# Kernel tuning notes

Measured on AMD Instinct MI355X. Metric: run time of the kernel, lower is better.

Reference implementation:

```python
import jax, jax.numpy as jnp
import numpy as np

IN_CH = 128
OUT_CH = 256
KSIZE = 3
DOWN = 2
WSCALE_GAIN = 1.0
LR_MUL = 1.0
ACT_GAIN = float(np.sqrt(2.0))  # lrelu def_gain
CONV_CLAMP = 256.0
LRELU_SLOPE = 0.2


def _setup_filter():
    # upfirdn2d.setup_filter([1,3,3,1]): normalize 1D then outer product -> 2D
    f1 = jnp.asarray([1.0, 3.0, 3.0, 1.0], dtype=jnp.float32)
    f1 = f1 / jnp.sum(f1)
    f2 = jnp.outer(f1, f1)  # [4,4]
    return f2


def setup_inputs() -> dict:
    key = jax.random.key(0)
    k1, k2 = jax.random.split(key)
    x = jax.random.normal(k1, (16, IN_CH, 256, 256), dtype=jnp.float32)
    weight = jax.random.normal(k2, (OUT_CH, IN_CH, KSIZE, KSIZE), dtype=jnp.float32)
    bias = jnp.zeros((OUT_CH,), dtype=jnp.float32)
    return {"x": x, "weight": weight, "bias": bias}


def reference(x, weight, bias):
    # runtime_gain = 1.0
    fan_in = KSIZE * KSIZE * IN_CH
    wscale = WSCALE_GAIN / np.sqrt(fan_in) * LR_MUL  # use_wscale=True
    w = weight * jnp.float32(wscale)
    b = bias * jnp.float32(LR_MUL)

    # filter_padding for k=3, fh=fw=4, down=2 -> (2,2,2,2) as (left,right,top,bottom)
    pad = (KSIZE // 2 + (4 - DOWN + 1) // 2, KSIZE // 2 + (4 - DOWN) // 2)
    # upfirdn2d(x, f, down=1, padding): pad then correlate with flipped filter
    f2 = _setup_filter()
    f2 = f2[::-1, ::-1]  # flip (symmetric here, kept for faithfulness)
    C = x.shape[1]
    fk = jnp.broadcast_to(f2[None, None], (C, 1, 4, 4))  # depthwise kernel
    x = lax.pad_fn(x, pad) if False else jnp.pad(x, ((0, 0), (0, 0), (pad[1], pad[0]) if False else (pad[0], pad[1]), (pad[0], pad[1])))
    x = jax.lax.conv_general_dilated(
        x, fk, window_strides=(1, 1), padding='VALID',
        dimension_numbers=('NCHW', 'OIHW', 'NCHW'),
        feature_group_count=C)

    # strided conv2d, padding=0, stride=down
    x = jax.lax.conv_general_dilated(
        x, w, window_strides=(DOWN, DOWN), padding='VALID',
        dimension_numbers=('NCHW', 'OIHW', 'NCHW'))

    # fused bias + lrelu + gain + clamp
    x = x + b[None, :, None, None]
    x = jnp.where(x >= 0, x, x * jnp.float32(LRELU_SLOPE)) * jnp.float32(ACT_GAIN)
    x = jnp.clip(x, -jnp.float32(CONV_CLAMP), jnp.float32(CONV_CLAMP))
    return x
```

## Files before the change

kernel.cpp:

```cpp
#include <hip/hip_runtime.h>

typedef __attribute__((ext_vector_type(8))) short bf16x8;
typedef __attribute__((ext_vector_type(4))) float f32x4;
typedef __attribute__((ext_vector_type(2))) float f32x2;
typedef __attribute__((ext_vector_type(4))) unsigned int u32x4;

static __device__ __forceinline__ unsigned short f2bf(float f) {
    union { float f; unsigned u; } v; v.f = f;
    return (unsigned short)((v.u + 0x7FFFu + ((v.u >> 16) & 1u)) >> 16);
}

static __device__ __forceinline__ void g2l16(const void* g, void* l) {
    __builtin_amdgcn_global_load_lds(
        (const __attribute__((address_space(1))) unsigned int*)g,
        (__attribute__((address_space(3))) unsigned int*)l, 16, 0, 0);
}

__global__ void prep_weights(const float* __restrict__ w, unsigned short* __restrict__ wp) {
    int t = blockIdx.x * 256 + threadIdx.x;
    const float wscale = 0.02946278254943948f;
    int cw = t & 31;
    int oc = (t >> 5) & 255;
    int cr = t >> 13;
    int ch = cr / 9;
    int rs = cr - ch * 9;
    int r  = rs / 3;
    int s  = rs - r * 3;
    int c  = ch * 32 + cw;
    wp[t] = f2bf(w[((oc * 128 + c) * 3 + r) * 3 + s] * wscale);
}

#define BRW(ROW) {                                                             \
    int _xr = xr0 + (ROW);                                                     \
    int _xc = _xr < 0 ? 0 : (_xr > 255 ? 255 : _xr);                           \
    float _rm = (_xr == _xc) ? 0.125f : 0.0f;                                  \
    const float* _q0 = p0lo + (_xc << 8);                                      \
    const float* _h0p = p0hi + (_xc << 8);                                     \
    const float* _q1 = p1lo + (_xc << 8);                                      \
    const float* _h1p = p1hi + (_xc << 8);                                     \
    f32x4 _l0, _l1; f32x2 _h0, _h1;                                            \
    __builtin_memcpy(&_l0, _q0, 16); __builtin_memcpy(&_h0, _h0p, 8);          \
    __builtin_memcpy(&_l1, _q1, 16); __builtin_memcpy(&_h1, _h1p, 8);          \
    float w00 = eL ? 0.f : _l0.x,  w01 = eL ? 0.f : _l0.y;                     \
    float w02 = eL ? _l0.x : _l0.z, w03 = eL ? _l0.y : _l0.w;                  \
    float w04 = eR ? 0.f : (eL ? _l0.z : _h0.x);                               \
    float w05 = eR ? 0.f : (eL ? _l0.w : _h0.y);                               \
    float w10 = eL ? 0.f : _l1.x,  w11 = eL ? 0.f : _l1.y;                     \
    float w12 = eL ? _l1.x : _l1.z, w13 = eL ? _l1.y : _l1.w;                  \
    float w14 = eR ? 0.f : (eL ? _l1.z : _h1.x);                               \
    float w15 = eR ? 0.f : (eL ? _l1.w : _h1.y);                               \
    hA0[(ROW) & 3] = (w00 + 3.f * (w01 + w02) + w03) * _rm;                    \
    hB0[(ROW) & 3] = (w01 + 3.f * (w02 + w03) + w04) * _rm;                    \
    hC0[(ROW) & 3] = (w02 + 3.f * (w03 + w04) + w05) * _rm;                    \
    hA1[(ROW) & 3] = (w10 + 3.f * (w11 + w12) + w13) * _rm;                    \
    hB1[(ROW) & 3] = (w11 + 3.f * (w12 + w13) + w14) * _rm;                    \
    hC1[(ROW) & 3] = (w12 + 3.f * (w13 + w14) + w15) * _rm;                    \
}
#define BWV(ROW, LBASE) {                                                      \
    float vA0 = (hA0[(ROW-3)&3] + 3.f*(hA0[(ROW-2)&3]+hA0[(ROW-1)&3]) + hA0[(ROW)&3]) * 0.125f; \
    float vA1 = (hA1[(ROW-3)&3] + 3.f*(hA1[(ROW-2)&3]+hA1[(ROW-1)&3]) + hA1[(ROW)&3]) * 0.125f; \
    float vB0 = (hB0[(ROW-3)&3] + 3.f*(hB0[(ROW-2)&3]+hB0[(ROW-1)&3]) + hB0[(ROW)&3]) * 0.125f; \
    float vB1 = (hB1[(ROW-3)&3] + 3.f*(hB1[(ROW-2)&3]+hB1[(ROW-1)&3]) + hB1[(ROW)&3]) * 0.125f; \
    unsigned _rb = (unsigned)(LBASE) * 2112u;                                  \
    *(unsigned*)(blds + _rb + o0) = (unsigned)f2bf(vA0) | ((unsigned)f2bf(vA1) << 16); \
    *(unsigned*)(blds + _rb + o1) = (unsigned)f2bf(vB0) | ((unsigned)f2bf(vB1) << 16); \
    if (a15) {                                                                 \
        float vC0 = (hC0[(ROW-3)&3] + 3.f*(hC0[(ROW-2)&3]+hC0[(ROW-1)&3]) + hC0[(ROW)&3]) * 0.125f; \
        float vC1 = (hC1[(ROW-3)&3] + 3.f*(hC1[(ROW-2)&3]+hC1[(ROW-1)&3]) + hC1[(ROW)&3]) * 0.125f; \
        *(unsigned*)(blds + _rb + o2) = (unsigned)f2bf(vC0) | ((unsigned)f2bf(vC1) << 16); \
    }                                                                          \
}

__global__ __launch_bounds__(256, 6)
void blur_rec(const float* __restrict__ x, unsigned char* __restrict__ bm) {
    __shared__ __align__(16) unsigned char blds[9 * 2112];

    const int braw = blockIdx.x;
    const int bx   = ((braw & 7) << 10) | (braw >> 3);
    const int cg   = bx & 3;
    const int tile = (bx >> 2) & 127;
    const int n    = bx >> 9;
    const int u0   = (tile >> 3) * 8;
    const int v0   = (tile & 7) * 16;
    const int tid  = threadIdx.x;
    const int a    = tid & 15;
    const int chp  = tid >> 4;
    const bool a15 = (a == 15);
    const int wc   = 2 * v0 - 2 + 2 * a;
    const bool eL  = (v0 == 0 && a == 0);
    const bool eR  = (v0 == 112 && a15);
    const int colLo = eL ? 0 : wc;
    const int colHi = eR ? 248 : (wc + 4);
    const float* plane0 = x + (size_t)(n * 128 + cg * 32 + 2 * chp) * 65536;
    const float* p0lo = plane0 + colLo;
    const float* p0hi = plane0 + colHi;
    const float* p1lo = p0lo + 65536;
    const float* p1hi = p0hi + 65536;
    const int xr0 = 2 * u0 - 2;

    const int J0 = 2 * a, J1 = 2 * a + 1;
    const unsigned cb2 = (unsigned)(chp & 3) * 4u;
    const unsigned o0 = (unsigned)((J0 ^ ((J0 >> 1) & 1)) * 64)
                      + ((((unsigned)chp >> 2) ^ (((unsigned)J0 >> 2) & 3u)) << 4) + cb2;
    const unsigned o1 = (unsigned)((J1 ^ ((J1 >> 1) & 1)) * 64)
                      + ((((unsigned)chp >> 2) ^ (((unsigned)J1 >> 2) & 3u)) << 4) + cb2;
    const unsigned o2 = 2048u + (((unsigned)chp >> 2) << 4) + cb2;

    unsigned char* dst = bm + (size_t)bx * 35904u;
    float hA0[4], hB0[4], hC0[4], hA1[4], hB1[4], hC1[4];

    BRW(0) BRW(1) BRW(2)
    BRW(3)  BWV(3, 0)   BRW(4)  BWV(4, 1)   BRW(5)  BWV(5, 2)
    BRW(6)  BWV(6, 3)   BRW(7)  BWV(7, 4)   BRW(8)  BWV(8, 5)
    BRW(9)  BWV(9, 6)   BRW(10) BWV(10, 7)  BRW(11) BWV(11, 8)
    __syncthreads();
    #pragma unroll
    for (int k = 0; k < 5; ++k) {
        int sl = tid + 256 * k;
        if (sl < 1188)
            *(u32x4*)(dst + (unsigned)sl * 16u) = *(const u32x4*)(blds + (unsigned)sl * 16u);
    }
    __syncthreads();
    BRW(12) BWV(12, 0)  BRW(13) BWV(13, 1)  BRW(14) BWV(14, 2)
    BRW(15) BWV(15, 3)  BRW(16) BWV(16, 4)  BRW(17) BWV(17, 5)
    BRW(18) BWV(18, 6)  BRW(19) BWV(19, 7)
    __syncthreads();
    unsigned char* dst2 = dst + 19008u;
    #pragma unroll
    for (int k = 0; k < 5; ++k) {
        int sl = tid + 256 * k;
        if (sl < 1056)
            *(u32x4*)(dst2 + (unsigned)sl * 16u) = *(const u32x4*)(blds + (unsigned)sl * 16u);
    }
}

#define MF __builtin_amdgcn_mfma_f32_16x16x32_bf16
#define WLOAD2(S0, S1, KOFF) {                                                 \
    const unsigned short* _wn = wbase + (size_t)(KOFF) * 8192;                 \
    S0 = *(const bf16x8*)(_wn); S1 = *(const bf16x8*)(_wn + 512);              \
}
#define CSTEP8(BUF, ADRS, R, S0, S1) {                                         \
    const unsigned char* _ab = lds + (BUF) + (ADRS) + (R) * 2112;              \
    bf16x8 a0 = *(const bf16x8*)(_ab);                                         \
    bf16x8 a1 = *(const bf16x8*)(_ab +  4224);                                 \
    bf16x8 a2 = *(const bf16x8*)(_ab +  8448);                                 \
    bf16x8 a3 = *(const bf16x8*)(_ab + 12672);                                 \
    bf16x8 a4 = *(const bf16x8*)(_ab + 16896);                                 \
    bf16x8 a5 = *(const bf16x8*)(_ab + 21120);                                 \
    bf16x8 a6 = *(const bf16x8*)(_ab + 25344);                                 \
    bf16x8 a7 = *(const bf16x8*)(_ab + 29568);                                 \
    __builtin_amdgcn_s_setprio(1);                                             \
    acc[0][0]=MF(a0,S0,acc[0][0],0,0,0); acc[0][1]=MF(a0,S1,acc[0][1],0,0,0);  \
    acc[1][0]=MF(a1,S0,acc[1][0],0,0,0); acc[1][1]=MF(a1,S1,acc[1][1],0,0,0);  \
    acc[2][0]=MF(a2,S0,acc[2][0],0,0,0); acc[2][1]=MF(a2,S1,acc[2][1],0,0,0);  \
    acc[3][0]=MF(a3,S0,acc[3][0],0,0,0); acc[3][1]=MF(a3,S1,acc[3][1],0,0,0);  \
    acc[4][0]=MF(a4,S0,acc[4][0],0,0,0); acc[4][1]=MF(a4,S1,acc[4][1],0,0,0);  \
    acc[5][0]=MF(a5,S0,acc[5][0],0,0,0); acc[5][1]=MF(a5,S1,acc[5][1],0,0,0);  \
    acc[6][0]=MF(a6,S0,acc[6][0],0,0,0); acc[6][1]=MF(a6,S1,acc[6][1],0,0,0);  \
    acc[7][0]=MF(a7,S0,acc[7][0],0,0,0); acc[7][1]=MF(a7,S1,acc[7][1],0,0,0);  \
    __builtin_amdgcn_s_setprio(0);                                             \
}
#define CHUNK8(BUF, BASE, A0,A1, B0,B1)                                        \
    CSTEP8(BUF, adr0, 0, A0,A1) WLOAD2(A0,A1, (BASE)+2)                        \
    CSTEP8(BUF, adr1, 0, B0,B1) WLOAD2(B0,B1, (BASE)+3)                        \
    CSTEP8(BUF, adr2, 0, A0,A1) WLOAD2(A0,A1, (BASE)+4)                        \
    CSTEP8(BUF, adr0, 1, B0,B1) WLOAD2(B0,B1, (BASE)+5)                        \
    CSTEP8(BUF, adr1, 1, A0,A1) WLOAD2(A0,A1, (BASE)+6)                        \
    CSTEP8(BUF, adr2, 1, B0,B1) WLOAD2(B0,B1, (BASE)+7)                        \
    CSTEP8(BUF, adr0, 2, A0,A1) WLOAD2(A0,A1, (BASE)+8)                        \
    CSTEP8(BUF, adr1, 2, B0,B1) WLOAD2(B0,B1, (BASE)+9)                        \
    CSTEP8(BUF, adr2, 2, A0,A1) WLOAD2(A0,A1, (BASE)+10)
#define CHUNK8_LAST(BUF, BASE, A0,A1, B0,B1)                                   \
    CSTEP8(BUF, adr0, 0, A0,A1) WLOAD2(A0,A1, (BASE)+2)                        \
    CSTEP8(BUF, adr1, 0, B0,B1) WLOAD2(B0,B1, (BASE)+3)                        \
    CSTEP8(BUF, adr2, 0, A0,A1) WLOAD2(A0,A1, (BASE)+4)                        \
    CSTEP8(BUF, adr0, 1, B0,B1) WLOAD2(B0,B1, (BASE)+5)                        \
    CSTEP8(BUF, adr1, 1, A0,A1) WLOAD2(A0,A1, (BASE)+6)                        \
    CSTEP8(BUF, adr2, 1, B0,B1) WLOAD2(B0,B1, (BASE)+7)                        \
    CSTEP8(BUF, adr0, 2, A0,A1) WLOAD2(A0,A1, (BASE)+8)                        \
    CSTEP8(BUF, adr1, 2, B0,B1)                                                \
    CSTEP8(BUF, adr2, 2, A0,A1)

__global__ __launch_bounds__(512, 4)
void conv_stage2(const unsigned char* __restrict__ bm, const unsigned short* __restrict__ wp,
                 const float* __restrict__ bias, float* __restrict__ out) {
    __shared__ __align__(16) unsigned char lds[2 * 35904];

    const int bx = blockIdx.x;
    const int n  = bx >> 7;
    const int tt = bx & 127;
    const int u0 = (tt >> 3) * 8;
    const int v0 = (tt & 7) * 16;

    const int tid  = threadIdx.x;
    const int lane = tid & 63;
    const int wid  = tid >> 6;
    const int g    = lane >> 4;
    const int wq   = lane & 15;

    const unsigned char* rec = bm + (size_t)((n * 128 + tt) * 4) * 35904u;

#define STAGE(BUF, CG) {                                                       \
    const unsigned char* _src = rec + (size_t)(CG) * 35904u;                   \
    _Pragma("unroll")                                                          \
    for (int k = 0; k < 4; ++k)                                                \
        g2l16(_src + (unsigned)(tid + 512 * k) * 16u,                          \
              lds + (BUF) + (unsigned)(tid + 512 * k) * 16u);                  \
    if (tid < 196)                                                             \
        g2l16(_src + (unsigned)(tid + 2048) * 16u,                             \
              lds + (BUF) + (unsigned)(tid + 2048) * 16u);                     \
}

    unsigned adr0, adr1, adr2;
    {
        #pragma unroll
        for (int s = 0; s < 3; ++s) {
            unsigned bj = 2u * (unsigned)wq + (unsigned)s;
            unsigned av = (bj ^ ((bj >> 1) & 1u)) * 64u
                        + (((unsigned)g ^ ((bj >> 2) & 3u)) << 4);
            if (s == 0) adr0 = av; else if (s == 1) adr1 = av; else adr2 = av;
        }
    }

    const unsigned short* wbase = wp + (size_t)(wid * 32 + wq) * 32 + g * 8;
    bf16x8 WA0, WA1, WB0, WB1;
    WLOAD2(WA0, WA1, 0)
    WLOAD2(WB0, WB1, 1)

    f32x4 acc[8][2];
    #pragma unroll
    for (int i = 0; i < 8; ++i) {
        acc[i][0] = (f32x4){0.f, 0.f, 0.f, 0.f};
        acc[i][1] = (f32x4){0.f, 0.f, 0.f, 0.f};
    }

    STAGE(0, 0)
    __syncthreads();

    STAGE(35904, 1)
    CHUNK8(0, 0, WA0, WA1, WB0, WB1)
    __syncthreads();

    STAGE(0, 2)
    CHUNK8(35904, 9, WB0, WB1, WA0, WA1)
    __syncthreads();

    STAGE(35904, 3)
    CHUNK8(0, 18, WA0, WA1, WB0, WB1)
    __syncthreads();

    CHUNK8_LAST(35904, 27, WB0, WB1, WA0, WA1)

    const float gain = 1.4142135623730951f;
    #pragma unroll
    for (int nf = 0; nf < 2; ++nf) {
        const int ocg = wid * 32 + nf * 16 + wq;
        const float bb = bias[ocg];
        #pragma unroll
        for (int mf = 0; mf < 8; ++mf) {
            f32x4 o;
            #pragma unroll
            for (int i = 0; i < 4; ++i) {
                float z = acc[mf][nf][i] + bb;
                z = (z >= 0.f ? z : 0.2f * z) * gain;
                o[i] = fminf(fmaxf(z, -256.f), 256.f);
            }
            *(f32x4*)(out + (((size_t)n * 256 + ocg) * 128 + (u0 + mf)) * 128 + v0 + 4 * g) = o;
        }
    }
}

#define FROW(row) {                                                            \
    int xr  = xr0 + (row);                                                     \
    int xrc = xr < 0 ? 0 : (xr > 255 ? 255 : xr);                              \
    float rm = (xr == xrc) ? 0.125f : 0.0f;                                    \
    const float* p = q + (xrc << 8);                                           \
    f32x4 lo; f32x2 hi;                                                        \
    __builtin_memcpy(&lo, p, 16);                                              \
    __builtin_memcpy(&hi, p + 4, 8);                                           \
    hA[(row) & 3] = (lo.x + 3.f * (lo.y + lo.z) + lo.w) * rm;                  \
    hB[(row) & 3] = (lo.y + 3.f * (lo.z + lo.w) + hi.x) * rm;                  \
    hC[(row) & 3] = (lo.z + 3.f * (lo.w + hi.x) + hi.y) * rm;                  \
}
#define SROW(row) {                                                            \
    int xr = xr0 + (row);                                                      \
    float wv0=0.f,wv1=0.f,wv2=0.f,wv3=0.f,wv4=0.f,wv5=0.f;                     \
    if ((unsigned)xr < 256u) {                                                 \
        const float* p = q + (xr << 8);                                        \
        if ((unsigned)(wc + 0) < 256u) wv0 = p[0];                             \
        if ((unsigned)(wc + 1) < 256u) wv1 = p[1];                             \
        if ((unsigned)(wc + 2) < 256u) wv2 = p[2];                             \
        if ((unsigned)(wc + 3) < 256u) wv3 = p[3];                             \
        if ((unsigned)(wc + 4) < 256u) wv4 = p[4];                             \
        if ((unsigned)(wc + 5) < 256u) wv5 = p[5];                             \
    }                                                                          \
    hA[(row) & 3] = (wv0 + 3.f * (wv1 + wv2) + wv3) * 0.125f;                  \
    hB[(row) & 3] = (wv1 + 3.f * (wv2 + wv3) + wv4) * 0.125f;                  \
    hC[(row) & 3] = (wv2 + 3.f * (wv3 + wv4) + wv5) * 0.125f;                  \
}
#define VROW(row) {                                                            \
    float bv0 = (hA[(row - 3) & 3] + 3.f * (hA[(row - 2) & 3] + hA[(row - 1) & 3]) + hA[(row) & 3]) * 0.125f; \
    float bv1 = (hB[(row - 3) & 3] + 3.f * (hB[(row - 2) & 3] + hB[(row - 1) & 3]) + hB[(row) & 3]) * 0.125f; \
    unsigned rb = (unsigned)(row - 3) * 2640u;                                 \
    *(unsigned short*)(flds + rb + o0) = f2bf(bv0);                            \
    *(unsigned short*)(flds + rb + o1) = f2bf(bv1);                            \
    if (a == 15) {                                                             \
        float bv2 = (hC[(row - 3) & 3] + 3.f * (hC[(row - 2) & 3] + hC[(row - 1) & 3]) + hC[(row) & 3]) * 0.125f; \
        *(unsigned short*)(flds + rb + o2) = f2bf(bv2);                        \
    }                                                                          \
}
__global__ __launch_bounds__(512, 4)
void conv_blur_mfma(const float* __restrict__ x, const unsigned short* __restrict__ wp,
                    const float* __restrict__ bias, float* __restrict__ out) {
    __shared__ __align__(16) unsigned char flds[17 * 33 * 80];
    const int bx = blockIdx.x;
    const int n  = bx >> 7;
    const int tt = bx & 127;
    const int u0 = (tt >> 3) * 8;
    const int v0 = (tt & 7) * 16;
    const int tid  = threadIdx.x;
    const int lane = tid & 63;
    const int wid  = tid >> 6;
    const int wm   = wid >> 2;
    const int wn   = wid & 3;
    const int g    = lane >> 4;
    const int wq   = lane & 15;
    const int a   = tid & 15;
    const int chl = tid >> 4;
    const int wc  = 2 * v0 - 2 + 2 * a;
    const bool edge = (v0 == 0 && a == 0) || (v0 == 112 && a == 15);
    const float* planeBase = x + (size_t)(n * 128 + chl) * 65536;
    const int xr0 = 2 * u0 - 2;
    const unsigned chpart = (unsigned)(((chl >> 1) & 3) * 4 + (chl & 1) * 2);
    const unsigned q4 = (unsigned)(chl >> 3);
    const int c0 = 2 * a;
    const unsigned o0 = (unsigned)(c0 + 0) * 80u + ((q4 ^ (((unsigned)(c0 + 0) >> 3) & 3u)) << 4) + chpart;
    const unsigned o1 = (unsigned)(c0 + 1) * 80u + ((q4 ^ (((unsigned)(c0 + 1) >> 3) & 3u)) << 4) + chpart;
    const unsigned o2 = (unsigned)(c0 + 2) * 80u + ((q4 ^ (((unsigned)(c0 + 2) >> 3) & 3u)) << 4) + chpart;
    const unsigned short* wpL = wp + (size_t)(wn * 64 + wq) * 32 + g * 8;
    f32x4 acc[4][4];
    #pragma unroll
    for (int i = 0; i < 4; ++i)
        #pragma unroll
        for (int j = 0; j < 4; ++j)
            acc[i][j] = (f32x4){0.f, 0.f, 0.f, 0.f};
    for (int ch = 0; ch < 4; ++ch) {
        const float* q = planeBase + (size_t)ch * 32 * 65536 + wc;
        float hA[4], hB[4], hC[4];
        if (!edge) { FROW(0) FROW(1) FROW(2) }
        else       { SROW(0) SROW(1) SROW(2) }
        __syncthreads();
        if (!edge) {
            #pragma unroll
            for (int row = 3; row < 20; ++row) { FROW(row) VROW(row) }
        } else {
            #pragma unroll
            for (int row = 3; row < 20; ++row) { SROW(row) VROW(row) }
        }
        __syncthreads();
        const unsigned short* wpc = wpL + (size_t)ch * 9 * 8192;
        #pragma unroll 1
        for (int r = 0; r < 3; ++r) {
            #pragma unroll 1
            for (int s = 0; s < 3; ++s) {
                bf16x8 b0 = *(const bf16x8*)(wpc + 0 * 512);
                bf16x8 b1 = *(const bf16x8*)(wpc + 1 * 512);
                bf16x8 b2 = *(const bf16x8*)(wpc + 2 * 512);
                bf16x8 b3 = *(const bf16x8*)(wpc + 3 * 512);
                wpc += 8192;
                int bj = 2 * wq + s;
                unsigned cb = (unsigned)bj * 80u + ((unsigned)(g ^ ((bj >> 3) & 3)) << 4);
                #pragma unroll
                for (int mf = 0; mf < 4; ++mf) {
                    int bi = 2 * (wm * 4 + mf) + r;
                    bf16x8 afrag = *(const bf16x8*)(flds + (unsigned)bi * 2640u + cb);
                    acc[mf][0] = MF(afrag, b0, acc[mf][0], 0, 0, 0);
                    acc[mf][1] = MF(afrag, b1, acc[mf][1], 0, 0, 0);
                    acc[mf][2] = MF(afrag, b2, acc[mf][2], 0, 0, 0);
                    acc[mf][3] = MF(afrag, b3, acc[mf][3], 0, 0, 0);
                }
            }
        }
    }
    const float gain = 1.4142135623730951f;
    #pragma unroll
    for (int nf = 0; nf < 4; ++nf) {
        int ocg = wn * 64 + nf * 16 + wq;
        float bv = bias[ocg];
        #pragma unroll
        for (int mf = 0; mf < 4; ++mf) {
            int u = u0 + wm * 4 + mf;
            f32x4 o;
            #pragma unroll
            for (int i = 0; i < 4; ++i) {
                float z = acc[mf][nf][i] + bv;
                z = (z >= 0.f ? z : 0.2f * z) * gain;
                o[i] = fminf(fmaxf(z, -256.f), 256.f);
            }
            *(f32x4*)(out + (((size_t)n * 256 + ocg) * 128 + u) * 128 + v0 + 4 * g) = o;
        }
    }
}

extern "C" void kernel_launch(void* const* d_in, const int* in_sizes, int n_in,
                              void* d_out, int out_size, void* d_ws, size_t ws_size,
                              hipStream_t stream) {
    const float* x    = (const float*)d_in[0];
    const float* w    = (const float*)d_in[1];
    const float* bias = (const float*)d_in[2];
    unsigned short* wp = (unsigned short*)d_ws;
    float* out = (float*)d_out;

    const size_t BM_BYTES = (size_t)8192 * 35904u;
    const size_t NEED = 589824u + BM_BYTES;
    prep_weights<<<1152, 256, 0, stream>>>(w, wp);
    if (ws_size >= NEED) {
        unsigned char* bm = (unsigned char*)d_ws + 589824;
        blur_rec<<<8192, 256, 0, stream>>>(x, bm);
        conv_stage2<<<2048, 512, 0, stream>>>(bm, wp, bias, out);
    } else {
        conv_blur_mfma<<<2048, 512, 0, stream>>>(x, wp, bias, out);
    }
}
```

Measured before the change: 413.5 us.

## Split blur row processing across two half-blocks with full-tile LDS staging

The blur pre-pass now launches 512 threads per block. The two halves of the block compute the first 9 and last 8 output rows of the tile in parallel, each recomputing a 3-row halo. LDS is enlarged to hold all 17 rows, so a single barrier and one copy-out replace the previous two sequential phases with their extra barriers. This adds redundant loads and horizontal filtering for the halo rows, and the larger LDS footprint and block size may lower occupancy.

```diff
diff --git a/kernel.cpp b/kernel.cpp
--- a/kernel.cpp
+++ b/kernel.cpp
@@ -56,12 +56,12 @@
     hB1[(ROW) & 3] = (w11 + 3.f * (w12 + w13) + w14) * _rm;                    \
     hC1[(ROW) & 3] = (w12 + 3.f * (w13 + w14) + w15) * _rm;                    \
 }
-#define BWV(ROW, LBASE) {                                                      \
+#define BWV(ROW) {                                                             \
     float vA0 = (hA0[(ROW-3)&3] + 3.f*(hA0[(ROW-2)&3]+hA0[(ROW-1)&3]) + hA0[(ROW)&3]) * 0.125f; \
     float vA1 = (hA1[(ROW-3)&3] + 3.f*(hA1[(ROW-2)&3]+hA1[(ROW-1)&3]) + hA1[(ROW)&3]) * 0.125f; \
     float vB0 = (hB0[(ROW-3)&3] + 3.f*(hB0[(ROW-2)&3]+hB0[(ROW-1)&3]) + hB0[(ROW)&3]) * 0.125f; \
     float vB1 = (hB1[(ROW-3)&3] + 3.f*(hB1[(ROW-2)&3]+hB1[(ROW-1)&3]) + hB1[(ROW)&3]) * 0.125f; \
-    unsigned _rb = (unsigned)(LBASE) * 2112u;                                  \
+    unsigned _rb = (unsigned)(ROW - 3) * 2112u;                                \
     *(unsigned*)(blds + _rb + o0) = (unsigned)f2bf(vA0) | ((unsigned)f2bf(vA1) << 16); \
     *(unsigned*)(blds + _rb + o1) = (unsigned)f2bf(vB0) | ((unsigned)f2bf(vB1) << 16); \
     if (a15) {                                                                 \
@@ -71,9 +71,9 @@
     }                                                                          \
 }
 
-__global__ __launch_bounds__(256, 6)
+__global__ __launch_bounds__(512, 4)
 void blur_rec(const float* __restrict__ x, unsigned char* __restrict__ bm) {
-    __shared__ __align__(16) unsigned char blds[9 * 2112];
+    __shared__ __align__(16) unsigned char blds[17 * 2112];
 
     const int braw = blockIdx.x;
     const int bx   = ((braw & 7) << 10) | (braw >> 3);
@@ -84,7 +84,8 @@
     const int v0   = (tile & 7) * 16;
     const int tid  = threadIdx.x;
     const int a    = tid & 15;
-    const int chp  = tid >> 4;
+    const int chp  = (tid >> 4) & 15;
+    const int h    = tid >> 8;
     const bool a15 = (a == 15);
     const int wc   = 2 * v0 - 2 + 2 * a;
     const bool eL  = (v0 == 0 && a == 0);
@@ -106,31 +107,27 @@
                       + ((((unsigned)chp >> 2) ^ (((unsigned)J1 >> 2) & 3u)) << 4) + cb2;
     const unsigned o2 = 2048u + (((unsigned)chp >> 2) << 4) + cb2;
 
+    {
+        float hA0[4], hB0[4], hC0[4], hA1[4], hB1[4], hC1[4];
+        if (h == 0) {
+            BRW(0) BRW(1) BRW(2)
+            BRW(3)  BWV(3)   BRW(4)  BWV(4)   BRW(5)  BWV(5)
+            BRW(6)  BWV(6)   BRW(7)  BWV(7)   BRW(8)  BWV(8)
+            BRW(9)  BWV(9)   BRW(10) BWV(10)  BRW(11) BWV(11)
+        } else {
+            BRW(9) BRW(10) BRW(11)
+            BRW(12) BWV(12)  BRW(13) BWV(13)  BRW(14) BWV(14)
+            BRW(15) BWV(15)  BRW(16) BWV(16)  BRW(17) BWV(17)
+            BRW(18) BWV(18)  BRW(19) BWV(19)
+        }
+    }
+    __syncthreads();
     unsigned char* dst = bm + (size_t)bx * 35904u;
-    float hA0[4], hB0[4], hC0[4], hA1[4], hB1[4], hC1[4];
-
-    BRW(0) BRW(1) BRW(2)
-    BRW(3)  BWV(3, 0)   BRW(4)  BWV(4, 1)   BRW(5)  BWV(5, 2)
-    BRW(6)  BWV(6, 3)   BRW(7)  BWV(7, 4)   BRW(8)  BWV(8, 5)
-    BRW(9)  BWV(9, 6)   BRW(10) BWV(10, 7)  BRW(11) BWV(11, 8)
-    __syncthreads();
     #pragma unroll
     for (int k = 0; k < 5; ++k) {
-        int sl = tid + 256 * k;
-        if (sl < 1188)
+        int sl = tid + 512 * k;
+        if (sl < 2244)
             *(u32x4*)(dst + (unsigned)sl * 16u) = *(const u32x4*)(blds + (unsigned)sl * 16u);
-    }
-    __syncthreads();
-    BRW(12) BWV(12, 0)  BRW(13) BWV(13, 1)  BRW(14) BWV(14, 2)
-    BRW(15) BWV(15, 3)  BRW(16) BWV(16, 4)  BRW(17) BWV(17, 5)
-    BRW(18) BWV(18, 6)  BRW(19) BWV(19, 7)
-    __syncthreads();
-    unsigned char* dst2 = dst + 19008u;
-    #pragma unroll
-    for (int k = 0; k < 5; ++k) {
-        int sl = tid + 256 * k;
-        if (sl < 1056)
-            *(u32x4*)(dst2 + (unsigned)sl * 16u) = *(const u32x4*)(blds + (unsigned)sl * 16u);
     }
 }
 
@@ -416,7 +413,7 @@
     prep_weights<<<1152, 256, 0, stream>>>(w, wp);
     if (ws_size >= NEED) {
         unsigned char* bm = (unsigned char*)d_ws + 589824;
-        blur_rec<<<8192, 256, 0, stream>>>(x, bm);
+        blur_rec<<<8192, 512, 0, stream>>>(x, bm);
         conv_stage2<<<2048, 512, 0, stream>>>(bm, wp, bias, out);
     } else {
         conv_blur_mfma<<<2048, 512, 0, stream>>>(x, wp, bias, out);
```

After: 421.3 us. Within noise of the previous version (+1.9%).
